# Kernel tuning notes

Hardware: AMD Instinct MI355X
Metric: run time of the kernel (lower is better)

The kernel has to match this reference:

```python
import jax, jax.numpy as jnp
import numpy as np

B, T, D = 4, 2048, 1024
H = 16
HD = D // H          # per-head dim (dk/heads = dv/heads = 64)
FF = 2048            # FFN default hidden_dim
EPS = 1e-5


def _ln(x, g, b):
    mu = jnp.mean(x, -1, keepdims=True)
    var = jnp.mean((x - mu) ** 2, -1, keepdims=True)
    return (x - mu) * jax.lax.rsqrt(var + EPS) * g + b


def setup_inputs() -> dict:
    key = jax.random.key(0)
    ks = jax.random.split(key, 12)
    s_in = 1.0 / np.sqrt(D)
    s_ff = 1.0 / np.sqrt(FF)
    return {
        "x": jax.random.normal(ks[0], (B, T, D), jnp.float32),
        # per-head projections stacked: [H, D, HD]
        "Wq": jax.random.uniform(ks[1], (H, D, HD), jnp.float32, -s_in, s_in),
        "bq": jnp.zeros((H, HD), jnp.float32),
        "Wk": jax.random.uniform(ks[2], (H, D, HD), jnp.float32, -s_in, s_in),
        "bk": jnp.zeros((H, HD), jnp.float32),
        "Wv": jax.random.uniform(ks[3], (H, D, HD), jnp.float32, -s_in, s_in),
        "bv": jnp.zeros((H, HD), jnp.float32),
        "Wo": jax.random.uniform(ks[4], (D, D), jnp.float32, -s_in, s_in),
        "bo": jnp.zeros((D,), jnp.float32),
        "ln1_g": jnp.ones((D,), jnp.float32),
        "ln1_b": jnp.zeros((D,), jnp.float32),
        "W1": jax.random.uniform(ks[5], (D, FF), jnp.float32, -s_in, s_in),
        "b1": jnp.zeros((FF,), jnp.float32),
        "W2": jax.random.uniform(ks[6], (FF, D), jnp.float32, -s_ff, s_ff),
        "b2": jnp.zeros((D,), jnp.float32),
        "ln2_g": jnp.ones((D,), jnp.float32),
        "ln2_b": jnp.zeros((D,), jnp.float32),
    }


def reference(x, Wq, bq, Wk, bk, Wv, bv, Wo, bo, ln1_g, ln1_b, W1, b1, W2, b2, ln2_g, ln2_b):
    # QKV projections (per-head Linear loop vectorized over H): [B,H,T,HD]
    q = jnp.einsum("btd,hdk->bhtk", x, Wq) + bq[:, None, :]
    k = jnp.einsum("btd,hdk->bhtk", x, Wk) + bk[:, None, :]
    v = jnp.einsum("btd,hdk->bhtk", x, Wv) + bv[:, None, :]
    # scaled dot-product attention; scale uses per-head dk = HD
    scores = jnp.einsum("bhtk,bhsk->bhts", q, k) / jnp.sqrt(jnp.float32(HD))
    weights = jax.nn.softmax(scores, axis=-1)
    ctx = jnp.einsum("bhts,bhsk->bhtk", weights, v)        # [B,H,T,HD]
    # concat heads along last dim (head order preserved) then output proj
    ctx = ctx.transpose(0, 2, 1, 3).reshape(B, T, D)
    c = ctx @ Wo + bo
    # residual + LayerNorm
    x = _ln(x + c, ln1_g, ln1_b)
    # FFN: Linear -> ReLU -> Linear
    y = jax.nn.relu(x @ W1 + b1) @ W2 + b2
    return _ln(x + y, ln2_g, ln2_b)
```

## Files before the change

### kernel.cpp

```cpp
#include <hip/hip_runtime.h>
#include <hip/hip_bf16.h>

#define BB 4
#define TT 2048
#define DD 1024
#define HH 16
#define HD 64
#define FF 2048
#define QSCL 0.1803368801111204f

typedef unsigned short u16;
typedef __bf16 bf16x8 __attribute__((ext_vector_type(8)));
typedef float f32x4 __attribute__((ext_vector_type(4)));
typedef float f32x16 __attribute__((ext_vector_type(16)));
typedef unsigned short u16x8 __attribute__((ext_vector_type(8)));
typedef unsigned short u16x4 __attribute__((ext_vector_type(4)));
typedef unsigned int u32x4 __attribute__((ext_vector_type(4)));

__device__ __forceinline__ u16 f2bf(float f) {
    return __builtin_bit_cast(u16, (__bf16)f);
}
__device__ __forceinline__ float bf2f(u16 u) {
    return __builtin_bit_cast(float, (unsigned)u << 16);
}
__device__ __forceinline__ float exp2fast(float x) {
    float r;
    asm("v_exp_f32 %0, %1" : "=v"(r) : "v"(x));
    return r;
}

__device__ __forceinline__ void gload16(const void* g, void* l) {
    __builtin_amdgcn_global_load_lds((const __attribute__((address_space(1))) void*)g,
                                     (__attribute__((address_space(3))) void*)l, 16, 0, 0);
}

__global__ __launch_bounds__(256) void convert_x(const float* __restrict__ in, u16* __restrict__ out, int n8) {
    int i = blockIdx.x * 256 + threadIdx.x;
    if (i >= n8) return;
    const float4* p = (const float4*)in + (size_t)i * 2;
    float4 a = p[0], b = p[1];
    u16x8 o;
    o[0] = f2bf(a.x); o[1] = f2bf(a.y); o[2] = f2bf(a.z); o[3] = f2bf(a.w);
    o[4] = f2bf(b.x); o[5] = f2bf(b.y); o[6] = f2bf(b.z); o[7] = f2bf(b.w);
    ((u16x8*)out)[i] = o;
}

__global__ __launch_bounds__(256) void transpose_conv(const float* __restrict__ in, u16* __restrict__ out, int R, int C) {
    __shared__ float tile[32][33];
    const int c0 = blockIdx.x * 32, r0 = blockIdx.y * 32;
    const int tx = threadIdx.x & 31, ty = threadIdx.x >> 5;
#pragma unroll
    for (int j = 0; j < 4; ++j) tile[ty + j * 8][tx] = in[(size_t)(r0 + ty + j * 8) * C + c0 + tx];
    __syncthreads();
#pragma unroll
    for (int j = 0; j < 4; ++j) out[(size_t)(c0 + ty + j * 8) * R + r0 + tx] = f2bf(tile[tx][ty + j * 8]);
}

__global__ __launch_bounds__(256) void qkv_transpose(const float* __restrict__ Wq, const float* __restrict__ Wk,
                                                     const float* __restrict__ Wv, u16* __restrict__ out) {
    __shared__ float tile[32][33];
    const int z = blockIdx.z, w = z >> 4, h = z & 15;
    const float* in = (w == 0 ? Wq : (w == 1 ? Wk : Wv)) + (size_t)h * (DD * HD);
    u16* op = out + (size_t)(w * 1024 + h * 64) * DD;
    const int c0 = blockIdx.x * 32, r0 = blockIdx.y * 32;
    const int tx = threadIdx.x & 31, ty = threadIdx.x >> 5;
#pragma unroll
    for (int j = 0; j < 4; ++j) tile[ty + j * 8][tx] = in[(size_t)(r0 + ty + j * 8) * HD + c0 + tx];
    __syncthreads();
#pragma unroll
    for (int j = 0; j < 4; ++j) op[(size_t)(c0 + ty + j * 8) * DD + r0 + tx] = f2bf(tile[tx][ty + j * 8]);
}

__global__ __launch_bounds__(256) void pack_bias(const float* __restrict__ bq, const float* __restrict__ bk,
                                                 const float* __restrict__ bv, float* __restrict__ out) {
    int i = blockIdx.x * 256 + threadIdx.x;
    if (i < 3072) {
        const float* s = i < 1024 ? bq : (i < 2048 ? bk : bv);
        out[i] = s[i & 1023];
    }
}

#define GBM 128
#define GBN 128
#define GBK 64

template <int EPI>
__global__ __launch_bounds__(256) void gemm_bt(const u16* __restrict__ A, const u16* __restrict__ Bt,
                                               const float* __restrict__ bias, const void* __restrict__ res,
                                               void* __restrict__ outp, void* __restrict__ outp2,
                                               int M, int N, int K) {
    __shared__ __align__(16) u16 sA[GBM * GBK];
    __shared__ __align__(16) u16 sB[GBN * GBK];
    const int t = threadIdx.x;
    const int lane = t & 63, wv = t >> 6;
    const int wm = (wv >> 1) * 64, wn = (wv & 1) * 64;
    const int lq = lane & 15, lk8 = (lane >> 4) * 8;
    const int nwg = gridDim.x * gridDim.y;
    const int bid = blockIdx.y * gridDim.x + blockIdx.x;
    const int swz = (bid & 7) * (nwg >> 3) + (bid >> 3);
    const int m0 = (swz / gridDim.x) * GBM, n0 = (swz % gridDim.x) * GBN;

    const int lr = lane >> 3, ch = lane & 7;
    const int colel = (ch ^ lr) << 3;
    const u16* Abase = A + (size_t)(m0 + wv * 32 + lr) * K + colel;
    const u16* Bbase = Bt + (size_t)(n0 + wv * 32 + lr) * K + colel;
    char* sAw = (char*)sA + wv * 32 * 128;
    char* sBw = (char*)sB + wv * 32 * 128;

    f32x4 acc[4][4];
#pragma unroll
    for (int i = 0; i < 4; ++i)
#pragma unroll
        for (int j = 0; j < 4; ++j) acc[i][j] = (f32x4){0.f, 0.f, 0.f, 0.f};

    for (int k0 = 0; k0 < K; k0 += GBK) {
#pragma unroll
        for (int i = 0; i < 4; ++i) {
            gload16(Abase + (size_t)i * 8 * K + k0, sAw + i * 1024);
            gload16(Bbase + (size_t)i * 8 * K + k0, sBw + i * 1024);
        }
        __syncthreads();
#pragma unroll
        for (int kk = 0; kk < 2; ++kk) {
            bf16x8 af[4], bfr[4];
#pragma unroll
            for (int mf = 0; mf < 4; ++mf) {
                int row = wm + mf * 16 + lq;
                int by = (row * 128 + kk * 64 + lk8 * 2) ^ ((row & 7) << 4);
                af[mf] = *(const bf16x8*)((const char*)sA + by);
            }
#pragma unroll
            for (int nf = 0; nf < 4; ++nf) {
                int row = wn + nf * 16 + lq;
                int by = (row * 128 + kk * 64 + lk8 * 2) ^ ((row & 7) << 4);
                bfr[nf] = *(const bf16x8*)((const char*)sB + by);
            }
#pragma unroll
            for (int mf = 0; mf < 4; ++mf)
#pragma unroll
                for (int nf = 0; nf < 4; ++nf)
                    acc[mf][nf] = __builtin_amdgcn_mfma_f32_16x16x32_bf16(af[mf], bfr[nf], acc[mf][nf], 0, 0, 0);
        }
        __syncthreads();
    }

    const int rbase = (lane >> 4) * 4;
#pragma unroll
    for (int mf = 0; mf < 4; ++mf) {
#pragma unroll
        for (int nf = 0; nf < 4; ++nf) {
            int gn = n0 + wn + nf * 16 + lq;
            float bv = bias[gn];
            if (EPI == 0) {
                int which = gn >> 10, hh = (gn >> 6) & 15, hd = gn & 63;
                int gm0 = m0 + wm + mf * 16 + rbase;
                int b = gm0 >> 11, tt2 = gm0 & 2047;
                if (which == 2) {
                    u16x4 pk;
#pragma unroll
                    for (int r = 0; r < 4; ++r) pk[r] = f2bf(acc[mf][nf][r] + bv);
                    *(u16x4*)((u16*)outp2 + ((size_t)(b * HH + hh) * HD + hd) * TT + tt2) = pk;
                } else {
                    float scl = (which == 0) ? QSCL : 1.f;
                    size_t off0 = (size_t)which * ((size_t)BB * HH * TT * HD) +
                                  ((size_t)(b * HH + hh) * TT + tt2) * HD + hd;
#pragma unroll
                    for (int r = 0; r < 4; ++r)
                        ((u16*)outp)[off0 + (size_t)r * HD] = f2bf((acc[mf][nf][r] + bv) * scl);
                }
            } else {
#pragma unroll
                for (int r = 0; r < 4; ++r) {
                    int gm = m0 + wm + mf * 16 + rbase + r;
                    size_t idx = (size_t)gm * N + gn;
                    float val = acc[mf][nf][r] + bv;
                    if (EPI == 2) {
                        ((u16*)outp)[idx] = f2bf(val > 0.f ? val : 0.f);
                    } else if (EPI == 1) {
                        ((u16*)outp)[idx] = f2bf(val + ((const float*)res)[idx]);
                    } else {
                        ((u16*)outp)[idx] = f2bf(val + bf2f(((const u16*)res)[idx]));
                    }
                }
            }
        }
    }
}

__global__ __launch_bounds__(256) void attn_kernel(const u16* __restrict__ qk, const u16* __restrict__ vt,
                                                   u16* __restrict__ ctx) {
    const int t = threadIdx.x, wv = t >> 6, lane = t & 63;
    const int l31 = lane & 31, hi = lane >> 5;
    const int lr = lane >> 3, ch = lane & 7;
    const int colel = (ch ^ lr) << 3;
    const int qt = blockIdx.x, bh = blockIdx.y;
    const size_t WSTR = (size_t)BB * HH * TT * HD;
    const u16* qp = qk + (size_t)bh * TT * HD;
    const u16* kp = qp + WSTR;
    const u16* vtp = vt + (size_t)bh * HD * TT;
    const int qr = qt * 128 + wv * 32;

    __shared__ __align__(16) u16 sK[64 * 64];
    __shared__ __align__(16) u16 sVt[64 * 64];

    const u16* kbase = kp + (size_t)(wv * 16 + lr) * HD + colel;
    const u16* vbase = vtp + (size_t)(wv * 16 + lr) * TT + colel;
    char* dK = (char*)sK + wv * 16 * 128;
    char* dV = (char*)sVt + wv * 16 * 128;

#define ATTN_STAGE(kb)                                                       \
    do {                                                                     \
        _Pragma("unroll") for (int ii = 0; ii < 2; ++ii) {                   \
            gload16(kbase + (size_t)((kb) + ii * 8) * HD, dK + ii * 1024);   \
            gload16(vbase + (size_t)(ii * 8) * TT + (kb), dV + ii * 1024);   \
        }                                                                    \
    } while (0)

    bf16x8 qf[4];
#pragma unroll
    for (int c = 0; c < 4; ++c)
        qf[c] = *(const bf16x8*)(qp + (size_t)(qr + l31) * HD + c * 16 + 8 * hi);

    int off[2][4];
#pragma unroll
    for (int half = 0; half < 2; ++half)
#pragma unroll
        for (int c = 0; c < 4; ++c) {
            int row = half * 32 + l31;
            off[half][c] = row * 128 + (((c * 16 + 8 * hi) * 2) ^ ((row & 7) << 4));
        }

    f32x16 psv = (f32x16)0.f;
    f32x16 oacc[2];
    oacc[0] = (f32x16)0.f;
    oacc[1] = (f32x16)0.f;

    ATTN_STAGE(0);

    const int NT = TT / 64;
    for (int kt = 0; kt < NT; ++kt) {
        __syncthreads();

        f32x16 sacc[2];
        sacc[0] = (f32x16)0.f;
        sacc[1] = (f32x16)0.f;
#pragma unroll
        for (int kb2 = 0; kb2 < 2; ++kb2)
#pragma unroll
            for (int c = 0; c < 4; ++c) {
                bf16x8 kf = *(const bf16x8*)((const char*)sK + off[kb2][c]);
                sacc[kb2] = __builtin_amdgcn_mfma_f32_32x32x16_bf16(kf, qf[c], sacc[kb2], 0, 0, 0);
            }

#pragma unroll
        for (int kb2 = 0; kb2 < 2; ++kb2) {
#pragma unroll
            for (int i = 0; i < 16; ++i) sacc[kb2][i] = exp2fast(sacc[kb2][i]);
            psv += sacc[kb2];
        }

        bf16x8 pfrag[4];
#pragma unroll
        for (int kb2 = 0; kb2 < 2; ++kb2)
#pragma unroll
            for (int c2 = 0; c2 < 2; ++c2) {
                const int base = c2 * 8;
                unsigned a0, a1, b0, b1;
                asm("v_cvt_pk_bf16_f32 %0, %1, %2" : "=v"(a0) : "v"(sacc[kb2][base + 0]), "v"(sacc[kb2][base + 1]));
                asm("v_cvt_pk_bf16_f32 %0, %1, %2" : "=v"(a1) : "v"(sacc[kb2][base + 2]), "v"(sacc[kb2][base + 3]));
                asm("v_cvt_pk_bf16_f32 %0, %1, %2" : "=v"(b0) : "v"(sacc[kb2][base + 4]), "v"(sacc[kb2][base + 5]));
                asm("v_cvt_pk_bf16_f32 %0, %1, %2" : "=v"(b1) : "v"(sacc[kb2][base + 6]), "v"(sacc[kb2][base + 7]));
                asm("v_permlane32_swap_b32 %0, %1" : "+v"(a0), "+v"(b0));
                asm("v_permlane32_swap_b32 %0, %1" : "+v"(a1), "+v"(b1));
                u32x4 w = {a0, a1, b0, b1};
                pfrag[kb2 * 2 + c2] = __builtin_bit_cast(bf16x8, w);
            }

#pragma unroll
        for (int db = 0; db < 2; ++db)
#pragma unroll
            for (int kc = 0; kc < 4; ++kc) {
                bf16x8 vf = *(const bf16x8*)((const char*)sVt + off[db][kc]);
                oacc[db] = __builtin_amdgcn_mfma_f32_32x32x16_bf16(vf, pfrag[kc], oacc[db], 0, 0, 0);
            }

        __syncthreads();
        if (kt + 1 < NT) ATTN_STAGE((kt + 1) * 64);
    }

    float ls = 0.f;
#pragma unroll
    for (int i = 0; i < 16; ++i) ls += psv[i];
    ls += __shfl_xor(ls, 32);
    const float inv = 1.f / ls;

    const int b = bh >> 4, h = bh & 15;
    u16* orow = ctx + ((size_t)b * TT + (qr + l31)) * DD + h * HD;
#pragma unroll
    for (int db = 0; db < 2; ++db)
#pragma unroll
        for (int rq = 0; rq < 4; ++rq) {
            u16x4 ov;
#pragma unroll
            for (int j = 0; j < 4; ++j) ov[j] = f2bf(oacc[db][rq * 4 + j] * inv);
            *(u16x4*)(orow + db * 32 + rq * 8 + 4 * hi) = ov;
        }
#undef ATTN_STAGE
}

template <bool OUTF32>
__global__ __launch_bounds__(256) void ln_kernel(const u16* __restrict__ y, const float* __restrict__ g,
                                                 const float* __restrict__ b, float* __restrict__ of,
                                                 u16* __restrict__ ob) {
    const int row = blockIdx.x, t = threadIdx.x;
    const u16x4 raw = *(const u16x4*)(y + (size_t)row * DD + t * 4);
    float v0 = bf2f(raw[0]), v1 = bf2f(raw[1]), v2 = bf2f(raw[2]), v3 = bf2f(raw[3]);
    float s = v0 + v1 + v2 + v3;
    float q = v0 * v0 + v1 * v1 + v2 * v2 + v3 * v3;
#pragma unroll
    for (int m = 1; m < 64; m <<= 1) {
        s += __shfl_xor(s, m);
        q += __shfl_xor(q, m);
    }
    __shared__ float red[8];
    const int wv = t >> 6, ln = t & 63;
    if (ln == 0) {
        red[wv] = s;
        red[4 + wv] = q;
    }
    __syncthreads();
    s = red[0] + red[1] + red[2] + red[3];
    q = red[4] + red[5] + red[6] + red[7];
    const float mu = s * (1.f / DD);
    const float var = q * (1.f / DD) - mu * mu;
    const float rstd = rsqrtf(var + 1e-5f);
    const float4 gg = ((const float4*)g)[t];
    const float4 bb = ((const float4*)b)[t];
    float o0 = (v0 - mu) * rstd * gg.x + bb.x;
    float o1 = (v1 - mu) * rstd * gg.y + bb.y;
    float o2 = (v2 - mu) * rstd * gg.z + bb.z;
    float o3 = (v3 - mu) * rstd * gg.w + bb.w;
    if (OUTF32) {
        ((float4*)(of + (size_t)row * DD))[t] = (float4){o0, o1, o2, o3};
    } else {
        u16x4 u;
        u[0] = f2bf(o0); u[1] = f2bf(o1); u[2] = f2bf(o2); u[3] = f2bf(o3);
        *(u16x4*)(ob + (size_t)row * DD + t * 4) = u;
    }
}

extern "C" void kernel_launch(void* const* d_in, const int* in_sizes, int n_in,
                              void* d_out, int out_size, void* d_ws, size_t ws_size,
                              hipStream_t stream) {
    const float* x   = (const float*)d_in[0];
    const float* Wq  = (const float*)d_in[1];
    const float* bq  = (const float*)d_in[2];
    const float* Wk  = (const float*)d_in[3];
    const float* bk  = (const float*)d_in[4];
    const float* Wv  = (const float*)d_in[5];
    const float* bv  = (const float*)d_in[6];
    const float* Wo  = (const float*)d_in[7];
    const float* bo  = (const float*)d_in[8];
    const float* g1  = (const float*)d_in[9];
    const float* be1 = (const float*)d_in[10];
    const float* W1  = (const float*)d_in[11];
    const float* b1  = (const float*)d_in[12];
    const float* W2  = (const float*)d_in[13];
    const float* b2  = (const float*)d_in[14];
    const float* g2  = (const float*)d_in[15];
    const float* be2 = (const float*)d_in[16];
    float* out = (float*)d_out;

    char* ws = (char*)d_ws;
    u16*   xb    = (u16*)(ws + 0);
    u16*   wqkvt = (u16*)(ws + 16777216);
    u16*   wot   = (u16*)(ws + 23068672);
    u16*   w1t   = (u16*)(ws + 25165824);
    u16*   w2t   = (u16*)(ws + 29360128);
    float* bqkv  = (float*)(ws + 33554432);
    u16*   qkb   = (u16*)(ws + 33566720);
    u16*   vtb   = qkb + (size_t)2 * BB * HH * TT * HD;
    u16*   y1b   = (u16*)(ws + 83898368);
    u16*   x1b   = (u16*)(ws + 100675584);
    u16*   ctx   = xb;
    u16*   hbuf  = qkb;
    u16*   y2b   = y1b;

    const int M = BB * TT;

    convert_x<<<dim3((M * DD / 8 + 255) / 256), 256, 0, stream>>>(x, xb, M * DD / 8);
    qkv_transpose<<<dim3(2, 32, 48), 256, 0, stream>>>(Wq, Wk, Wv, wqkvt);
    transpose_conv<<<dim3(32, 32), 256, 0, stream>>>(Wo, wot, DD, DD);
    transpose_conv<<<dim3(64, 32), 256, 0, stream>>>(W1, w1t, DD, FF);
    transpose_conv<<<dim3(32, 64), 256, 0, stream>>>(W2, w2t, FF, DD);
    pack_bias<<<dim3(12), 256, 0, stream>>>(bq, bk, bv, bqkv);

    gemm_bt<0><<<dim3(3 * DD / GBN, M / GBM), 256, 0, stream>>>(xb, wqkvt, bqkv, nullptr, qkb, vtb, M, 3 * DD, DD);
    attn_kernel<<<dim3(TT / 128, BB * HH), 256, 0, stream>>>(qkb, vtb, ctx);
    gemm_bt<1><<<dim3(DD / GBN, M / GBM), 256, 0, stream>>>(ctx, wot, bo, x, y1b, nullptr, M, DD, DD);
    ln_kernel<false><<<dim3(M), 256, 0, stream>>>(y1b, g1, be1, nullptr, x1b);
    gemm_bt<2><<<dim3(FF / GBN, M / GBM), 256, 0, stream>>>(x1b, w1t, b1, nullptr, hbuf, nullptr, M, FF, DD);
    gemm_bt<3><<<dim3(DD / GBN, M / GBM), 256, 0, stream>>>(hbuf, w2t, b2, x1b, y2b, nullptr, M, DD, FF);
    ln_kernel<true><<<dim3(M), 256, 0, stream>>>(y2b, g2, be2, out, nullptr);
}
```

Measured before the change: 318.0 us.

## Double-buffer attention K/V tiles and widen blocks to 8 waves

The attention kernel now uses 512 threads (8 waves, 256 query rows per block) and keeps two shared-memory buffers for the K and V^T tiles. The next tile is prefetched into the alternate buffer before the current one is computed, and explicit vmcnt waits plus raw barriers replace the old sync-then-load sequence, so global loads overlap the MFMA work. Doubling the rows per block also halves the number of K/V tile reloads across blocks. In exchange the block uses more LDS and registers per block and there are half as many blocks, which may lower occupancy. The hand-written waitcnt has to match the async load count exactly to stay correct.

```diff
diff --git a/kernel.cpp b/kernel.cpp
--- a/kernel.cpp
+++ b/kernel.cpp
@@ -187,7 +187,7 @@
     }
 }
 
-__global__ __launch_bounds__(256) void attn_kernel(const u16* __restrict__ qk, const u16* __restrict__ vt,
+__global__ __launch_bounds__(512) void attn_kernel(const u16* __restrict__ qk, const u16* __restrict__ vt,
                                                    u16* __restrict__ ctx) {
     const int t = threadIdx.x, wv = t >> 6, lane = t & 63;
     const int l31 = lane & 31, hi = lane >> 5;
@@ -198,22 +198,20 @@
     const u16* qp = qk + (size_t)bh * TT * HD;
     const u16* kp = qp + WSTR;
     const u16* vtp = vt + (size_t)bh * HD * TT;
-    const int qr = qt * 128 + wv * 32;
-
-    __shared__ __align__(16) u16 sK[64 * 64];
-    __shared__ __align__(16) u16 sVt[64 * 64];
-
-    const u16* kbase = kp + (size_t)(wv * 16 + lr) * HD + colel;
-    const u16* vbase = vtp + (size_t)(wv * 16 + lr) * TT + colel;
-    char* dK = (char*)sK + wv * 16 * 128;
-    char* dV = (char*)sVt + wv * 16 * 128;
-
-#define ATTN_STAGE(kb)                                                       \
-    do {                                                                     \
-        _Pragma("unroll") for (int ii = 0; ii < 2; ++ii) {                   \
-            gload16(kbase + (size_t)((kb) + ii * 8) * HD, dK + ii * 1024);   \
-            gload16(vbase + (size_t)(ii * 8) * TT + (kb), dV + ii * 1024);   \
-        }                                                                    \
+    const int qr = qt * 256 + wv * 32;
+
+    __shared__ __align__(16) u16 sK[2][64 * 64];
+    __shared__ __align__(16) u16 sVt[2][64 * 64];
+
+    const u16* kbase = kp + (size_t)(wv * 8 + lr) * HD + colel;
+    const u16* vbase = vtp + (size_t)(wv * 8 + lr) * TT + colel;
+    char* dK = (char*)sK + wv * 1024;
+    char* dV = (char*)sVt + wv * 1024;
+
+#define ATTN_STAGE(bufi, kb)                                        \
+    do {                                                            \
+        gload16(kbase + (size_t)(kb)*HD, dK + (bufi)*8192);         \
+        gload16(vbase + (kb), dV + (bufi)*8192);                    \
     } while (0)
 
     bf16x8 qf[4];
@@ -235,11 +233,22 @@
     oacc[0] = (f32x16)0.f;
     oacc[1] = (f32x16)0.f;
 
-    ATTN_STAGE(0);
+    ATTN_STAGE(0, 0);
 
     const int NT = TT / 64;
     for (int kt = 0; kt < NT; ++kt) {
-        __syncthreads();
+        const int cur = kt & 1;
+        if (kt + 1 < NT) {
+            ATTN_STAGE(cur ^ 1, (kt + 1) * 64);
+            asm volatile("s_waitcnt vmcnt(2)" ::: "memory");
+        } else {
+            asm volatile("s_waitcnt vmcnt(0)" ::: "memory");
+        }
+        __builtin_amdgcn_s_barrier();
+        __builtin_amdgcn_sched_barrier(0);
+
+        const char* sKc = (const char*)sK + cur * 8192;
+        const char* sVc = (const char*)sVt + cur * 8192;
 
         f32x16 sacc[2];
         sacc[0] = (f32x16)0.f;
@@ -248,7 +257,7 @@
         for (int kb2 = 0; kb2 < 2; ++kb2)
 #pragma unroll
             for (int c = 0; c < 4; ++c) {
-                bf16x8 kf = *(const bf16x8*)((const char*)sK + off[kb2][c]);
+                bf16x8 kf = *(const bf16x8*)(sKc + off[kb2][c]);
                 sacc[kb2] = __builtin_amdgcn_mfma_f32_32x32x16_bf16(kf, qf[c], sacc[kb2], 0, 0, 0);
             }
 
@@ -280,12 +289,12 @@
         for (int db = 0; db < 2; ++db)
 #pragma unroll
             for (int kc = 0; kc < 4; ++kc) {
-                bf16x8 vf = *(const bf16x8*)((const char*)sVt + off[db][kc]);
+                bf16x8 vf = *(const bf16x8*)(sVc + off[db][kc]);
                 oacc[db] = __builtin_amdgcn_mfma_f32_32x32x16_bf16(vf, pfrag[kc], oacc[db], 0, 0, 0);
             }
 
-        __syncthreads();
-        if (kt + 1 < NT) ATTN_STAGE((kt + 1) * 64);
+        __builtin_amdgcn_sched_barrier(0);
+        __builtin_amdgcn_s_barrier();
     }
 
     float ls = 0.f;
@@ -396,7 +405,7 @@
     pack_bias<<<dim3(12), 256, 0, stream>>>(bq, bk, bv, bqkv);
 
     gemm_bt<0><<<dim3(3 * DD / GBN, M / GBM), 256, 0, stream>>>(xb, wqkvt, bqkv, nullptr, qkb, vtb, M, 3 * DD, DD);
-    attn_kernel<<<dim3(TT / 128, BB * HH), 256, 0, stream>>>(qkb, vtb, ctx);
+    attn_kernel<<<dim3(TT / 256, BB * HH), 512, 0, stream>>>(qkb, vtb, ctx);
     gemm_bt<1><<<dim3(DD / GBN, M / GBM), 256, 0, stream>>>(ctx, wot, bo, x, y1b, nullptr, M, DD, DD);
     ln_kernel<false><<<dim3(M), 256, 0, stream>>>(y1b, g1, be1, nullptr, x1b);
     gemm_bt<2><<<dim3(FF / GBN, M / GBM), 256, 0, stream>>>(x1b, w1t, b1, nullptr, hbuf, nullptr, M, FF, DD);
```

Measured after the change: 302.4 us. 1.05x faster.
